# Performance work log

Measured on AMD Instinct MI355X. Metric: run time of the kernel, lower is better.

## Reference

```python
import jax, jax.numpy as jnp
import numpy as np

NUM_VIEWS = 8
GAMMA = 10.0
EPS = 1e-06
B, LMAX, D = 16, 4096, 1024


def setup_inputs() -> dict:
    key = jax.random.key(0)
    k1, k2, k3 = jax.random.split(key, 3)
    v_pad = jax.random.normal(k1, (B, LMAX, D), dtype=jnp.float32)
    centers = jax.random.uniform(k2, (B, NUM_VIEWS, 2), dtype=jnp.float32)
    # per-sample grid sizes: H, W in [32, 64) so L = H*W <= LMAX (64*64 padding)
    hw = jax.random.randint(k3, (B, 2), 32, 64, dtype=jnp.int32)
    grid_thws = jnp.concatenate([jnp.ones((B, 1), jnp.int32), hw], axis=1)  # [B, 3] = (t, H, W)
    v_len = (hw[:, 0] * hw[:, 1]).astype(jnp.int32)
    return {"v_pad": v_pad, "centers": centers, "v_len": v_len, "grid_thws": grid_thws}


def reference(v_pad, centers, v_len, grid_thws):
    # v_pad: [B, Lmax, D]; centers: [B, V, 2]; grid_thws: [B, 3] ints (t, H, W)
    Lmax = v_pad.shape[1]
    H = grid_thws[:, 1]  # [B]
    W = grid_thws[:, 2]  # [B]
    l = jnp.arange(Lmax, dtype=jnp.int32)  # [L] row-major index into the HxW grid
    i = l[None, :] // W[:, None]           # [B, L] grid row
    j = l[None, :] % W[:, None]            # [B, L] grid col
    y = (i.astype(v_pad.dtype) + 0.5) / H[:, None].astype(v_pad.dtype)
    x = (j.astype(v_pad.dtype) + 0.5) / W[:, None].astype(v_pad.dtype)
    valid = (l[None, :] < (H * W)[:, None])  # [B, L] mask padded rows
    coords = jnp.stack([x, y], axis=-1)      # [B, L, 2] (x, y) as in torch code
    diff = centers[:, :, None, :] - coords[:, None, :, :]   # [B, V, L, 2]
    dist_sq = jnp.sum(diff * diff, axis=-1)                 # [B, V, L]
    m = jnp.exp(-GAMMA * dist_sq) * valid[:, None, :].astype(v_pad.dtype)
    numerator = jnp.einsum('bvl,bld->bvd', m, v_pad)        # [B, V, D]
    denominator = jnp.sum(m, axis=-1, keepdims=True) + EPS  # [B, V, 1]
    return numerator / denominator
```

## Files before the change

kernel.cpp:

```cpp
#include <hip/hip_runtime.h>

#define NV 8
#define NB 16
#define LMAX 4096
#define ND 1024
#define CHUNK 64
#define NCHUNK (LMAX / CHUNK)
#define EPS_ 1e-6f
#define NEXP10 (-14.426950408889634f)

#define PNUM_FLOATS ((size_t)NB * NCHUNK * NV * ND)

__global__ __launch_bounds__(256, 4) void dvs_accum(
    const float* __restrict__ v_pad,
    const float* __restrict__ centers,
    const int* __restrict__ grid_thws,
    float* __restrict__ pnum,
    float* __restrict__ pden)
{
    const int b     = blockIdx.x >> 6;
    const int chunk = blockIdx.x & (NCHUNK - 1);
    const int H  = grid_thws[b * 3 + 1];
    const int W  = grid_thws[b * 3 + 2];
    const int HW = H * W;
    const int l0 = chunk * CHUNK;
    if (l0 >= HW) return;

    __shared__ __align__(16) float wlds[CHUNK][NV];

    const int t = threadIdx.x;

    const float4* __restrict__ src =
        (const float4*)v_pad + ((size_t)b * LMAX + l0) * (ND / 4) + t;
    float4 c0 = src[0 * 256];
    float4 c1 = src[1 * 256];
    float4 c2 = src[2 * 256];
    float4 c3 = src[3 * 256];

    const float invH = 1.0f / (float)H;
    const float invW = 1.0f / (float)W;
#pragma unroll
    for (int g = 0; g < 2; ++g) {
        const int idx = t + g * 256;
        const int row = idx >> 3;
        const int v   = idx & 7;
        const int l   = l0 + row;
        const int i   = l / W;
        const int j   = l - i * W;
        const float y = ((float)i + 0.5f) * invH;
        const float x = ((float)j + 0.5f) * invW;
        const float2 c = ((const float2*)centers)[b * NV + v];
        const float dx = c.x - x;
        const float dy = c.y - y;
        const float s  = fmaf(dy, dy, dx * dx);
        wlds[row][v] = (l < HW) ? exp2f(s * NEXP10) : 0.0f;
    }
    __syncthreads();

    const size_t pbase = (size_t)(b * NCHUNK + chunk) * NV;
    if (t < NV) {
        float s = 0.0f;
#pragma unroll
        for (int r = 0; r < CHUNK; ++r) s += wlds[r][t];
        pden[pbase + t] = s;
    }

    float acc[NV][4];
#pragma unroll
    for (int v = 0; v < NV; ++v)
#pragma unroll
        for (int k = 0; k < 4; ++k) acc[v][k] = 0.0f;

    auto proc = [&](const int r, const float4 r4) {
        float w[NV];
        *(float4*)&w[0] = *(const float4*)&wlds[r][0];
        *(float4*)&w[4] = *(const float4*)&wlds[r][4];
#pragma unroll
        for (int v = 0; v < NV; ++v) {
            acc[v][0] = fmaf(w[v], r4.x, acc[v][0]);
            acc[v][1] = fmaf(w[v], r4.y, acc[v][1]);
            acc[v][2] = fmaf(w[v], r4.z, acc[v][2]);
            acc[v][3] = fmaf(w[v], r4.w, acc[v][3]);
        }
    };

    for (int r = 0; r < CHUNK; r += 4) {
        float4 n0 = c0, n1 = c1, n2 = c2, n3 = c3;
        if (r + 4 < CHUNK) {
            n0 = src[(r + 4) * 256];
            n1 = src[(r + 5) * 256];
            n2 = src[(r + 6) * 256];
            n3 = src[(r + 7) * 256];
        }
        proc(r + 0, c0); proc(r + 1, c1); proc(r + 2, c2); proc(r + 3, c3);
        c0 = n0; c1 = n1; c2 = n2; c3 = n3;
    }

    float4* np_ = (float4*)pnum;
#pragma unroll
    for (int v = 0; v < NV; ++v)
        np_[(pbase + v) * (ND / 4) + t] =
            make_float4(acc[v][0], acc[v][1], acc[v][2], acc[v][3]);
}

__global__ __launch_bounds__(64) void dvs_reduce(
    const float* __restrict__ pnum,
    const float* __restrict__ pden,
    const int* __restrict__ grid_thws,
    float* __restrict__ out)
{
    const int bv = blockIdx.x >> 2;
    const int q  = blockIdx.x & 3;
    const int b  = bv >> 3;
    const int v  = bv & (NV - 1);
    const int HW = grid_thws[b * 3 + 1] * grid_thws[b * 3 + 2];
    const int nc = (HW + CHUNK - 1) / CHUNK;
    const int t  = threadIdx.x;
    const int f4 = q * 64 + t;

    const float4* np_ = (const float4*)pnum;
    const size_t cstride = (size_t)NV * (ND / 4);
    const size_t base = ((size_t)b * NCHUNK * NV + v) * (ND / 4) + f4;
    const int dbase = b * NCHUNK * NV + v;

    float4 s0 = make_float4(0.f, 0.f, 0.f, 0.f), s1 = s0, s2 = s0, s3 = s0;
    float d0 = 0.f, d1 = 0.f, d2 = 0.f, d3 = 0.f;
    int c = 0;
    for (; c + 4 <= nc; c += 4) {
        float4 p0 = np_[base + (size_t)(c + 0) * cstride];
        float4 p1 = np_[base + (size_t)(c + 1) * cstride];
        float4 p2 = np_[base + (size_t)(c + 2) * cstride];
        float4 p3 = np_[base + (size_t)(c + 3) * cstride];
        d0 += pden[dbase + (c + 0) * NV];
        d1 += pden[dbase + (c + 1) * NV];
        d2 += pden[dbase + (c + 2) * NV];
        d3 += pden[dbase + (c + 3) * NV];
        s0.x += p0.x; s0.y += p0.y; s0.z += p0.z; s0.w += p0.w;
        s1.x += p1.x; s1.y += p1.y; s1.z += p1.z; s1.w += p1.w;
        s2.x += p2.x; s2.y += p2.y; s2.z += p2.z; s2.w += p2.w;
        s3.x += p3.x; s3.y += p3.y; s3.z += p3.z; s3.w += p3.w;
    }
    for (; c < nc; ++c) {
        float4 p0 = np_[base + (size_t)c * cstride];
        d0 += pden[dbase + c * NV];
        s0.x += p0.x; s0.y += p0.y; s0.z += p0.z; s0.w += p0.w;
    }
    const float inv = 1.0f / (d0 + d1 + d2 + d3 + EPS_);
    float4 o = make_float4((s0.x + s1.x + s2.x + s3.x) * inv,
                           (s0.y + s1.y + s2.y + s3.y) * inv,
                           (s0.z + s1.z + s2.z + s3.z) * inv,
                           (s0.w + s1.w + s2.w + s3.w) * inv);
    ((float4*)out)[(size_t)bv * (ND / 4) + f4] = o;
}

extern "C" void kernel_launch(void* const* d_in, const int* in_sizes, int n_in,
                              void* d_out, int out_size, void* d_ws, size_t ws_size,
                              hipStream_t stream) {
    const float* v_pad     = (const float*)d_in[0];
    const float* centers   = (const float*)d_in[1];
    const int*   grid_thws = (const int*)d_in[3];

    float* pnum = (float*)d_ws;
    float* pden = pnum + PNUM_FLOATS;

    dvs_accum<<<NB * NCHUNK, 256, 0, stream>>>(v_pad, centers, grid_thws, pnum, pden);
    dvs_reduce<<<NB * NV * 4, 64, 0, stream>>>(pnum, pden, grid_thws, (float*)d_out);
}
```

Measured before the change: 35.94 us.

## Deepen load prefetch, interleave batches across blocks, parallelize denominator sum

```diff
diff --git a/kernel.cpp b/kernel.cpp
--- a/kernel.cpp
+++ b/kernel.cpp
@@ -18,8 +18,9 @@
     float* __restrict__ pnum,
     float* __restrict__ pden)
 {
-    const int b     = blockIdx.x >> 6;
-    const int chunk = blockIdx.x & (NCHUNK - 1);
+    const int bid   = blockIdx.x;
+    const int b     = bid & (NB - 1);
+    const int chunk = bid >> 4;
     const int H  = grid_thws[b * 3 + 1];
     const int W  = grid_thws[b * 3 + 2];
     const int HW = H * W;
@@ -32,10 +33,14 @@
 
     const float4* __restrict__ src =
         (const float4*)v_pad + ((size_t)b * LMAX + l0) * (ND / 4) + t;
-    float4 c0 = src[0 * 256];
-    float4 c1 = src[1 * 256];
-    float4 c2 = src[2 * 256];
-    float4 c3 = src[3 * 256];
+    float4 a0 = src[0 * 256];
+    float4 a1 = src[1 * 256];
+    float4 a2 = src[2 * 256];
+    float4 a3 = src[3 * 256];
+    float4 b0 = src[4 * 256];
+    float4 b1 = src[5 * 256];
+    float4 b2 = src[6 * 256];
+    float4 b3 = src[7 * 256];
 
     const float invH = 1.0f / (float)H;
     const float invW = 1.0f / (float)W;
@@ -58,11 +63,16 @@
     __syncthreads();
 
     const size_t pbase = (size_t)(b * NCHUNK + chunk) * NV;
-    if (t < NV) {
+    if (t < 64) {
+        const int rg = t >> 3;
+        const int v  = t & 7;
         float s = 0.0f;
 #pragma unroll
-        for (int r = 0; r < CHUNK; ++r) s += wlds[r][t];
-        pden[pbase + t] = s;
+        for (int k = 0; k < 8; ++k) s += wlds[rg + 8 * k][v];
+        s += __shfl_xor(s, 8);
+        s += __shfl_xor(s, 16);
+        s += __shfl_xor(s, 32);
+        if (rg == 0) pden[pbase + v] = s;
     }
 
     float acc[NV][4];
@@ -84,16 +94,26 @@
         }
     };
 
-    for (int r = 0; r < CHUNK; r += 4) {
-        float4 n0 = c0, n1 = c1, n2 = c2, n3 = c3;
-        if (r + 4 < CHUNK) {
-            n0 = src[(r + 4) * 256];
-            n1 = src[(r + 5) * 256];
-            n2 = src[(r + 6) * 256];
-            n3 = src[(r + 7) * 256];
+#pragma unroll
+    for (int r = 0; r < CHUNK; r += 8) {
+        float4 n0 = a0, n1 = a1, n2 = a2, n3 = a3;
+        if (r + 8 < CHUNK) {
+            n0 = src[(r + 8)  * 256];
+            n1 = src[(r + 9)  * 256];
+            n2 = src[(r + 10) * 256];
+            n3 = src[(r + 11) * 256];
         }
-        proc(r + 0, c0); proc(r + 1, c1); proc(r + 2, c2); proc(r + 3, c3);
-        c0 = n0; c1 = n1; c2 = n2; c3 = n3;
+        proc(r + 0, a0); proc(r + 1, a1); proc(r + 2, a2); proc(r + 3, a3);
+        float4 m0 = b0, m1 = b1, m2 = b2, m3 = b3;
+        if (r + 12 < CHUNK) {
+            m0 = src[(r + 12) * 256];
+            m1 = src[(r + 13) * 256];
+            m2 = src[(r + 14) * 256];
+            m3 = src[(r + 15) * 256];
+        }
+        proc(r + 4, b0); proc(r + 5, b1); proc(r + 6, b2); proc(r + 7, b3);
+        a0 = n0; a1 = n1; a2 = n2; a3 = n3;
+        b0 = m0; b1 = m1; b2 = m2; b3 = m3;
     }
 
     float4* np_ = (float4*)pnum;
```

New measurement: 36.24 us. About the same (+0.8%).
